# Kernel tuning notes

Hardware: AMD Instinct MI355X
Metric: run time of the kernel (lower is better)

The kernel has to match this reference:

```python
import jax, jax.numpy as jnp
import numpy as np

B, N, DIM = 4, 2048, 256
HEADS, CODEBOOK, HD = 4, 8192, 64  # HD = DIM // HEADS


def setup_inputs() -> dict:
    key = jax.random.key(0)
    k1, k2 = jax.random.split(key)
    x = jax.random.normal(k1, (B, N, DIM), dtype=jnp.float32)
    embed = jax.random.normal(k2, (HEADS, CODEBOOK, HD), dtype=jnp.float32)
    return {"x": x, "embed": embed}


def reference(x, embed):
    b, n, dim = x.shape
    h, c, d = embed.shape
    # 'b n (h d) -> h b n d' then pack to 'h (b n) d'
    flat = x.reshape(b, n, h, d).transpose(2, 0, 1, 3).reshape(h, b * n, d)
    x2 = jnp.sum(flat * flat, axis=-1)              # [h, bn]
    y2 = jnp.sum(embed * embed, axis=-1)            # [h, c]
    xy = jnp.einsum('hmd,hcd->hmc', flat, embed)    # [h, bn, c]
    sq = x2[:, :, None] + y2[:, None, :] - 2.0 * xy
    dist = -jnp.sqrt(jnp.maximum(sq, 0.0))          # clamp for fp safety
    embed_ind = jnp.argmax(dist, axis=-1)           # [h, bn]
    # gather codes per head
    quantize = jnp.take_along_axis(embed, embed_ind[:, :, None], axis=1)  # [h, bn, d]
    # 'h (b n) d -> b n (h d)'
    quantize = quantize.reshape(h, b, n, d).transpose(1, 2, 0, 3).reshape(b, n, h * d)
    # 'h (b n) -> b n h'
    embed_ind = embed_ind.reshape(h, b, n).transpose(1, 2, 0)
    return quantize, embed_ind
```

## Files before the change

kernel.cpp:

```cpp
#include <hip/hip_runtime.h>
#include <hip/hip_bf16.h>


#define HEADS    4
#define CODEBOOK 8192
#define HD       64
#define BQ       8192
#define QOFF     (4 * 2048 * 256)
#define NPART    8
#define CPART    (CODEBOOK / NPART)
#define SCODES   64
#define NSTAGE   (CPART / SCODES)
#define RSCALE   4096.0f
#define RINV     (1.0f / 4096.0f)

typedef _Float16 f16x8 __attribute__((ext_vector_type(8)));
typedef float    f32x4 __attribute__((ext_vector_type(4)));

__device__ float g_pval[NPART][HEADS * BQ];
__device__ int   g_pidx[NPART][HEADS * BQ];

__device__ inline void split2(float f, _Float16& h0, _Float16& h1) {
    h0 = (_Float16)f;
    float r = f - (float)h0;
    h1 = (_Float16)(r * RSCALE);
}

__global__ __launch_bounds__(256, 2) void dist_kernel(const float* __restrict__ x,
                                                      const float* __restrict__ embed) {
    __shared__ __align__(16) _Float16 tile[2][2][SCODES * 64];
    __shared__ float y2s[CPART];

    const int bid  = blockIdx.x;
    const int part = bid & 7;
    const int qg   = (bid >> 3) & 31;
    const int h    = bid >> 8;
    const int t    = threadIdx.x;
    const int wave = t >> 6;
    const int lane = t & 63;
    const int col  = lane & 15;
    const int quad = lane >> 4;

    const int qbase = qg * 256 + wave * 64;
    const int cbase = part * CPART;

    f16x8 a[4][2][2];
#pragma unroll
    for (int rt = 0; rt < 4; rt++) {
#pragma unroll
        for (int kh = 0; kh < 2; kh++) {
            const float* p = x + ((size_t)(qbase + rt * 16 + col) * 256 + h * 64 + kh * 32 + quad * 8);
#pragma unroll
            for (int j = 0; j < 8; j++) {
                _Float16 h0, h1;
                split2(p[j], h0, h1);
                a[rt][0][kh][j] = h0;
                a[rt][1][kh][j] = h1;
            }
        }
    }

    const float* esrc = embed + ((size_t)h * CODEBOOK + cbase) * HD + (size_t)t * 8;
    const int row  = t >> 3;
    const int gsw  = (t & 7) ^ (row & 7);
    const int ldA  = row * 64 + gsw * 8;
    const int ldB  = (row + 32) * 64 + gsw * 8;

    float bv[4][4]; int bc[4][4];
#pragma unroll
    for (int rt = 0; rt < 4; rt++)
#pragma unroll
        for (int r = 0; r < 4; r++) { bv[rt][r] = -3.4e38f; bc[rt][r] = 0; }

    float4 pfA0, pfA1, pfB0, pfB1;

    auto stage_write = [&](int buf, int stage) {
        float fA[8] = {pfA0.x, pfA0.y, pfA0.z, pfA0.w, pfA1.x, pfA1.y, pfA1.z, pfA1.w};
        float fB[8] = {pfB0.x, pfB0.y, pfB0.z, pfB0.w, pfB1.x, pfB1.y, pfB1.z, pfB1.w};
        f16x8 vA0, vA1, vB0, vB1;
        float ssA = 0.f, ssB = 0.f;
#pragma unroll
        for (int j = 0; j < 8; j++) {
            _Float16 h0, h1;
            split2(fA[j], h0, h1);
            vA0[j] = h0; vA1[j] = h1;
            ssA = fmaf(fA[j], fA[j], ssA);
            split2(fB[j], h0, h1);
            vB0[j] = h0; vB1[j] = h1;
            ssB = fmaf(fB[j], fB[j], ssB);
        }
        *reinterpret_cast<f16x8*>(&tile[buf][0][ldA]) = vA0;
        *reinterpret_cast<f16x8*>(&tile[buf][1][ldA]) = vA1;
        *reinterpret_cast<f16x8*>(&tile[buf][0][ldB]) = vB0;
        *reinterpret_cast<f16x8*>(&tile[buf][1][ldB]) = vB1;
#pragma unroll
        for (int off = 4; off >= 1; off >>= 1) {
            ssA += __shfl_xor(ssA, off, 8);
            ssB += __shfl_xor(ssB, off, 8);
        }
        if ((t & 7) == 0) {
            y2s[stage * SCODES + row]      = -0.5f * ssA;
            y2s[stage * SCODES + row + 32] = -0.5f * ssB;
        }
    };
    auto stage_load = [&](int stage) {
        const float* ps = esrc + (size_t)stage * (SCODES * HD);
        pfA0 = *reinterpret_cast<const float4*>(ps);
        pfA1 = *reinterpret_cast<const float4*>(ps + 4);
        pfB0 = *reinterpret_cast<const float4*>(ps + 32 * HD);
        pfB1 = *reinterpret_cast<const float4*>(ps + 32 * HD + 4);
    };

    stage_load(0);
    stage_write(0, 0);
    stage_load(1);
    __syncthreads();

    const int swbase = col & 7;

    for (int s = 0; s < NSTAGE; s++) {
        if (s + 1 < NSTAGE) stage_write((s + 1) & 1, s + 1);
        if (s + 2 < NSTAGE) stage_load(s + 2);

#pragma unroll
        for (int inner = 0; inner < 4; inner++) {
            const int rbase = (inner * 16 + col) * 64;
            f16x8 b[2][2];
#pragma unroll
            for (int lvl = 0; lvl < 2; lvl++)
#pragma unroll
                for (int kh = 0; kh < 2; kh++)
                    b[lvl][kh] = *reinterpret_cast<const f16x8*>(
                        &tile[s & 1][lvl][rbase + ((((kh << 2) | quad) ^ swbase) << 3)]);

            const int   c   = s * SCODES + inner * 16 + col;
            const float ycn = y2s[c];
#pragma unroll
            for (int rt = 0; rt < 4; rt++) {
                f32x4 aA = {ycn, ycn, ycn, ycn};
                f32x4 aB = {0.f, 0.f, 0.f, 0.f};
#pragma unroll
                for (int kh = 0; kh < 2; kh++) {
                    aA = __builtin_amdgcn_mfma_f32_16x16x32_f16(a[rt][0][kh], b[0][kh], aA, 0, 0, 0);
                    aB = __builtin_amdgcn_mfma_f32_16x16x32_f16(a[rt][0][kh], b[1][kh], aB, 0, 0, 0);
                    aB = __builtin_amdgcn_mfma_f32_16x16x32_f16(a[rt][1][kh], b[0][kh], aB, 0, 0, 0);
                }
#pragma unroll
                for (int r = 0; r < 4; r++) {
                    float sv = fmaf(aB[r], RINV, aA[r]);
                    if (sv > bv[rt][r]) { bv[rt][r] = sv; bc[rt][r] = c; }
                }
            }
        }
        __syncthreads();
    }

#pragma unroll
    for (int rt = 0; rt < 4; rt++) {
#pragma unroll
        for (int r = 0; r < 4; r++) {
            float v = bv[rt][r]; int c = bc[rt][r];
#pragma unroll
            for (int off = 8; off >= 1; off >>= 1) {
                float ov = __shfl_xor(v, off, 16); int oc = __shfl_xor(c, off, 16);
                if (ov > v || (ov == v && oc < c)) { v = ov; c = oc; }
            }
            if (col == 0) {
                int q = h * BQ + qbase + rt * 16 + quad * 4 + r;
                g_pval[part][q] = v; g_pidx[part][q] = cbase + c;
            }
        }
    }
}

__global__ __launch_bounds__(256) void merge_kernel(const float* __restrict__ embed,
                                                    float* __restrict__ out) {
    int id = blockIdx.x * 256 + threadIdx.x;
    int m = id >> 2;
    int h = id & 3;
    int q = h * BQ + m;

    float bv = g_pval[0][q]; int bc = g_pidx[0][q];
#pragma unroll
    for (int p = 1; p < NPART; p++) {
        float v = g_pval[p][q]; int c = g_pidx[p][q];
        if (v > bv || (v == bv && c < bc)) { bv = v; bc = c; }
    }

    out[QOFF + id] = (float)bc;

    int idx = bc & (CODEBOOK - 1);
    const float* src = embed + ((size_t)h * CODEBOOK + idx) * HD;
    float*       dst = out + (size_t)m * 256 + h * 64;
#pragma unroll
    for (int i = 0; i < 16; i++)
        *reinterpret_cast<float4*>(dst + i * 4) = *reinterpret_cast<const float4*>(src + i * 4);
}

extern "C" void kernel_launch(void* const* d_in, const int* in_sizes, int n_in,
                              void* d_out, int out_size, void* d_ws, size_t ws_size,
                              hipStream_t stream) {
    const float* x     = (const float*)d_in[0];
    const float* embed = (const float*)d_in[1];
    float*       out   = (float*)d_out;

    dist_kernel <<<1024, 256, 0, stream>>>(x, embed);
    merge_kernel<<<128,  256, 0, stream>>>(embed, out);
}
```

Measured before the change: 190.0 us.

## Reorder MFMA chains with setprio and coalesce merge gather writes

In the distance kernel, the MFMA sequence is reordered so the two accumulators are interleaved with zero-initialized starts. It is wrapped in s_setprio to favour matrix issue, and the y2 bias is added after the MFMAs instead of seeding the accumulator. The merge kernel now stages winning indices in shared memory and has each wave copy whole 256-float output rows with coalesced float4 accesses, using twice as many blocks. This targets strided per-thread gather writes in the merge and MFMA dependency stalls, at the cost of an extra add per element and a block-level sync.

```diff
diff --git a/kernel.cpp b/kernel.cpp
--- a/kernel.cpp
+++ b/kernel.cpp
@@ -117,6 +117,7 @@
     __syncthreads();
 
     const int swbase = col & 7;
+    const f32x4 z4 = {0.f, 0.f, 0.f, 0.f};
 
     for (int s = 0; s < NSTAGE; s++) {
         if (s + 1 < NSTAGE) stage_write((s + 1) & 1, s + 1);
@@ -137,17 +138,17 @@
             const float ycn = y2s[c];
 #pragma unroll
             for (int rt = 0; rt < 4; rt++) {
-                f32x4 aA = {ycn, ycn, ycn, ycn};
-                f32x4 aB = {0.f, 0.f, 0.f, 0.f};
-#pragma unroll
-                for (int kh = 0; kh < 2; kh++) {
-                    aA = __builtin_amdgcn_mfma_f32_16x16x32_f16(a[rt][0][kh], b[0][kh], aA, 0, 0, 0);
-                    aB = __builtin_amdgcn_mfma_f32_16x16x32_f16(a[rt][0][kh], b[1][kh], aB, 0, 0, 0);
-                    aB = __builtin_amdgcn_mfma_f32_16x16x32_f16(a[rt][1][kh], b[0][kh], aB, 0, 0, 0);
-                }
+                __builtin_amdgcn_s_setprio(1);
+                f32x4 aA = __builtin_amdgcn_mfma_f32_16x16x32_f16(a[rt][0][0], b[0][0], z4, 0, 0, 0);
+                f32x4 aB = __builtin_amdgcn_mfma_f32_16x16x32_f16(a[rt][0][0], b[1][0], z4, 0, 0, 0);
+                aB = __builtin_amdgcn_mfma_f32_16x16x32_f16(a[rt][1][0], b[0][0], aB, 0, 0, 0);
+                aA = __builtin_amdgcn_mfma_f32_16x16x32_f16(a[rt][0][1], b[0][1], aA, 0, 0, 0);
+                aB = __builtin_amdgcn_mfma_f32_16x16x32_f16(a[rt][0][1], b[1][1], aB, 0, 0, 0);
+                aB = __builtin_amdgcn_mfma_f32_16x16x32_f16(a[rt][1][1], b[0][1], aB, 0, 0, 0);
+                __builtin_amdgcn_s_setprio(0);
 #pragma unroll
                 for (int r = 0; r < 4; r++) {
-                    float sv = fmaf(aB[r], RINV, aA[r]);
+                    float sv = fmaf(aB[r], RINV, aA[r] + ycn);
                     if (sv > bv[rt][r]) { bv[rt][r] = sv; bc[rt][r] = c; }
                 }
             }
@@ -175,26 +176,38 @@
 
 __global__ __launch_bounds__(256) void merge_kernel(const float* __restrict__ embed,
                                                     float* __restrict__ out) {
-    int id = blockIdx.x * 256 + threadIdx.x;
-    int m = id >> 2;
-    int h = id & 3;
-    int q = h * BQ + m;
-
-    float bv = g_pval[0][q]; int bc = g_pidx[0][q];
-#pragma unroll
-    for (int p = 1; p < NPART; p++) {
-        float v = g_pval[p][q]; int c = g_pidx[p][q];
-        if (v > bv || (v == bv && c < bc)) { bv = v; bc = c; }
-    }
-
-    out[QOFF + id] = (float)bc;
-
-    int idx = bc & (CODEBOOK - 1);
-    const float* src = embed + ((size_t)h * CODEBOOK + idx) * HD;
-    float*       dst = out + (size_t)m * 256 + h * 64;
-#pragma unroll
-    for (int i = 0; i < 16; i++)
-        *reinterpret_cast<float4*>(dst + i * 4) = *reinterpret_cast<const float4*>(src + i * 4);
+    __shared__ int iw[32][4];
+    const int t     = threadIdx.x;
+    const int mbase = blockIdx.x * 32;
+
+    if (t < 128) {
+        const int ml = t >> 2;
+        const int h  = t & 3;
+        const int q  = h * BQ + mbase + ml;
+        float bv = g_pval[0][q]; int bc = g_pidx[0][q];
+#pragma unroll
+        for (int p = 1; p < NPART; p++) {
+            float v = g_pval[p][q]; int c = g_pidx[p][q];
+            if (v > bv || (v == bv && c < bc)) { bv = v; bc = c; }
+        }
+        out[QOFF + (size_t)mbase * 4 + t] = (float)bc;
+        iw[ml][h] = bc & (CODEBOOK - 1);
+    }
+    __syncthreads();
+
+    const int wave = t >> 6;
+    const int lane = t & 63;
+    const int h    = lane >> 4;
+    const int off  = (lane & 15) * 4;
+#pragma unroll
+    for (int i = 0; i < 8; i++) {
+        const int r   = wave * 8 + i;
+        const int m   = mbase + r;
+        const int idx = iw[r][h];
+        const float4 v = *reinterpret_cast<const float4*>(
+            embed + ((size_t)h * CODEBOOK + idx) * HD + off);
+        *reinterpret_cast<float4*>(out + (size_t)m * 256 + lane * 4) = v;
+    }
 }
 
 extern "C" void kernel_launch(void* const* d_in, const int* in_sizes, int n_in,
@@ -205,5 +218,5 @@
     float*       out   = (float*)d_out;
 
     dist_kernel <<<1024, 256, 0, stream>>>(x, embed);
-    merge_kernel<<<128,  256, 0, stream>>>(embed, out);
-}
+    merge_kernel<<<256,  256, 0, stream>>>(embed, out);
+}
```

New measurement: 178.8 us. 5.9% less time.
